# Kernel optimization log

Hardware: AMD Instinct MI355X
Metric: run time of the kernel (lower is better)

## Reference

```python
import jax, jax.numpy as jnp
import numpy as np


def setup_inputs() -> dict:
    key = jax.random.key(0)
    ks = jax.random.split(key, 6)
    B, C, H, W = 4, 512, 64, 64
    Ci = C // 2
    x = jax.random.normal(ks[0], (B, C, H, W), dtype=jnp.float32)
    # 1x1 conv weights (kaiming-ish scale)
    wq = jax.random.normal(ks[1], (Ci, C), dtype=jnp.float32) * np.float32(np.sqrt(2.0 / C))
    wk = jax.random.normal(ks[2], (Ci, C), dtype=jnp.float32) * np.float32(np.sqrt(2.0 / C))
    wv = jax.random.normal(ks[3], (C, C), dtype=jnp.float32) * np.float32(np.sqrt(2.0 / C))
    bq = jnp.zeros((Ci,), jnp.float32)
    bk = jnp.zeros((Ci,), jnp.float32)
    bv = jnp.zeros((C,), jnp.float32)
    gamma_pam = jax.random.uniform(ks[4], (1,), dtype=jnp.float32)
    gamma_cam = jax.random.uniform(ks[5], (1,), dtype=jnp.float32)
    return {"x": x, "wq": wq, "bq": bq, "wk": wk, "bk": bk,
            "wv": wv, "bv": bv, "gamma_pam": gamma_pam, "gamma_cam": gamma_cam}


def reference(x, wq, bq, wk, bk, wv, bv, gamma_pam, gamma_cam):
    B, C, H, W = x.shape
    N = H * W
    xf = x.reshape(B, C, N)  # [B,C,N]

    # ---- PAM (position attention) ----
    q = jnp.einsum('oc,bcn->bon', wq, xf) + bq[None, :, None]  # [B,C/2,N]
    k = jnp.einsum('oc,bcn->bon', wk, xf) + bk[None, :, None]  # [B,C/2,N]
    v = jnp.einsum('oc,bcn->bon', wv, xf) + bv[None, :, None]  # [B,C,N]
    # energy[b,i,j] = sum_c q[b,c,i] k[b,c,j] / sqrt(C)
    energy = jnp.einsum('bci,bcj->bij', q, k) / jnp.sqrt(jnp.float32(C))
    attn = jax.nn.softmax(energy, axis=-1) / jnp.float32(N)  # [B,N,N]
    # out[b,c,i] = sum_j v[b,c,j] * attn[i,j]
    pam_out = jnp.einsum('bcj,bij->bci', v, attn)
    sa = jnp.tanh(gamma_pam[0] * pam_out + xf)  # [B,C,N]

    # ---- CAM (channel attention) on sa ----
    energy_c = jnp.einsum('bcn,bdn->bcd', sa, sa) / jnp.sqrt(jnp.float32(N))  # [B,C,C]
    energy_new = jnp.max(energy_c, axis=-1, keepdims=True) - energy_c
    attn_c = jax.nn.softmax(energy_new, axis=-1) / jnp.float32(C)
    cam_out = jnp.einsum('bcd,bdn->bcn', attn_c, sa)
    out = gamma_cam[0] * cam_out + sa
    return out.reshape(B, C, H, W)
```

## Files before the change

kernel.cpp:

```cpp
#include <hip/hip_runtime.h>

#define B_ 4
#define C_ 512
#define CI_ 256
#define N_ 4096
#define SCALE_PAM 0.04419417382415922f
#define SCALE_CAM (1.0f/64.0f)
#define SHIFT_PAM 8.0f

typedef float v4f __attribute__((ext_vector_type(4)));
typedef short v8s __attribute__((ext_vector_type(8)));

__device__ __forceinline__ unsigned short f2bf(float f) {
  unsigned int u = __float_as_uint(f);
  u = (u + 0x7FFFu + ((u >> 16) & 1u)) >> 16;
  return (unsigned short)u;
}
__device__ __forceinline__ float bf2f(unsigned short s) {
  return __uint_as_float(((unsigned int)s) << 16);
}
__device__ __forceinline__ v8s ld8(const unsigned short* p) {
  v8s r; *(int4*)&r = *(const int4*)p; return r;
}
__device__ __forceinline__ v4f mfma16(v8s a, v8s b, v4f c) {
  return __builtin_amdgcn_mfma_f32_16x16x32_bf16(a, b, c, 0, 0, 0);
}

__global__ __launch_bounds__(256) void k_wb(const float* __restrict__ wq,
                                            const float* __restrict__ wk,
                                            const float* __restrict__ wv,
                                            unsigned short* __restrict__ w_pk) {
  int u = blockIdx.x * 256 + threadIdx.x;
  int blk = u >> 6, wi = (u & 63) * 8;
  int r = (blk >> 4) * 16 + (wi >> 5);
  int k = (blk & 15) * 32 + (wi & 31);
  const float* src = (r < 256) ? &wq[r * 512 + k]
                   : (r < 512) ? &wk[(r - 256) * 512 + k]
                               : &wv[(r - 512) * 512 + k];
  float4 f0 = *(const float4*)src, f1 = *(const float4*)(src + 4);
  ushort4 o0 = { f2bf(f0.x), f2bf(f0.y), f2bf(f0.z), f2bf(f0.w) };
  ushort4 o1 = { f2bf(f1.x), f2bf(f1.y), f2bf(f1.z), f2bf(f1.w) };
  *(ushort4*)&w_pk[u * 8] = o0;
  *(ushort4*)&w_pk[u * 8 + 4] = o1;
}

__global__ __launch_bounds__(256) void k_xT(const float* __restrict__ x,
                                            unsigned short* __restrict__ x_pk) {
  const int b = blockIdx.z, c0 = blockIdx.y * 64, n0 = blockIdx.x * 64;
  const int t = threadIdx.x;
  __shared__ unsigned short ts[64 * 72];
  const int cl = t >> 2, nseg = (t & 3) * 16;
  const float* xr = x + ((size_t)b * C_ + c0 + cl) * N_ + n0 + nseg;
#pragma unroll
  for (int k = 0; k < 4; ++k) {
    float4 f = *(const float4*)(xr + k * 4);
    ts[(nseg + k * 4 + 0) * 72 + cl] = f2bf(f.x);
    ts[(nseg + k * 4 + 1) * 72 + cl] = f2bf(f.y);
    ts[(nseg + k * 4 + 2) * 72 + cl] = f2bf(f.z);
    ts[(nseg + k * 4 + 3) * 72 + cl] = f2bf(f.w);
  }
  __syncthreads();
  unsigned short* dst = x_pk + (size_t)b * N_ * C_;
#pragma unroll
  for (int u = t; u < 512; u += 256) {
    int blk = u >> 6, wi = (u & 63) * 8;
    int rl = (blk >> 1) * 16 + (wi >> 5);
    int kl = (blk & 1) * 32 + (wi & 31);
    int gr = n0 + rl, gk = c0 + kl;
    size_t go = ((size_t)(gr >> 4) * 16 + (gk >> 5)) * 512 + (gr & 15) * 32 + (gk & 31);
    *(int4*)&dst[go] = *(int4*)&ts[rl * 72 + kl];
  }
}

__global__ __launch_bounds__(512) void k_qkv(
    const unsigned short* __restrict__ w_pk, const unsigned short* __restrict__ x_pk,
    const float* __restrict__ bq, const float* __restrict__ bk, const float* __restrict__ bv,
    unsigned short* __restrict__ q_pk, unsigned short* __restrict__ k_pk,
    unsigned short* __restrict__ v_pk) {
  const int b = blockIdx.z, o0 = blockIdx.y * 128, n0 = blockIdx.x * 128;
  const int t = threadIdx.x, wave = t >> 6, lane = t & 63;
  const int la = lane & 15, quad = lane >> 4;
  const int ow = wave & 1, nw = wave >> 1;
  const int lanelin = la * 32 + quad * 8;
  const unsigned short* xpb = x_pk + (size_t)b * N_ * C_;
  __shared__ unsigned short tp[128 * 136];

  v4f acc[4][2];
#pragma unroll
  for (int i = 0; i < 4; ++i)
#pragma unroll
    for (int j = 0; j < 2; ++j) acc[i][j] = (v4f){0.f, 0.f, 0.f, 0.f};

  const int ar16 = (o0 + ow * 64) >> 4;
  const int br16 = (n0 + nw * 32) >> 4;
#pragma unroll 4
  for (int s = 0; s < 16; ++s) {
    v8s b0 = ld8(&xpb[((size_t)(br16 + 0) * 16 + s) * 512 + lanelin]);
    v8s b1 = ld8(&xpb[((size_t)(br16 + 1) * 16 + s) * 512 + lanelin]);
#pragma unroll
    for (int oi = 0; oi < 4; ++oi) {
      v8s a = ld8(&w_pk[((size_t)(ar16 + oi) * 16 + s) * 512 + lanelin]);
      acc[oi][0] = mfma16(a, b0, acc[oi][0]);
      acc[oi][1] = mfma16(a, b1, acc[oi][1]);
    }
  }

  if (o0 >= 512) {
#pragma unroll
    for (int oi = 0; oi < 4; ++oi)
#pragma unroll
      for (int nj = 0; nj < 2; ++nj)
#pragma unroll
        for (int r = 0; r < 4; ++r) {
          int cl = ow * 64 + oi * 16 + quad * 4 + r;
          int nl = nw * 32 + nj * 16 + la;
          tp[cl * 136 + nl] = f2bf(acc[oi][nj][r] + bv[o0 - 512 + cl]);
        }
    __syncthreads();
    unsigned short* dst = v_pk + (size_t)b * C_ * N_;
#pragma unroll
    for (int u = t; u < 2048; u += 512) {
      int blk = u >> 6, wi = (u & 63) * 8;
      int rl = (blk >> 2) * 16 + (wi >> 5);
      int kl = (blk & 3) * 32 + (wi & 31);
      int gr = (o0 - 512) + rl, gk = n0 + kl;
      size_t go = ((size_t)(gr >> 4) * 128 + (gk >> 5)) * 512 + (gr & 15) * 32 + (gk & 31);
      *(int4*)&dst[go] = *(int4*)&tp[rl * 136 + kl];
    }
  } else {
    const float* bias = (o0 < 256) ? bq : bk;
#pragma unroll
    for (int oi = 0; oi < 4; ++oi)
#pragma unroll
      for (int nj = 0; nj < 2; ++nj)
#pragma unroll
        for (int r = 0; r < 4; ++r) {
          int ol = ow * 64 + oi * 16 + quad * 4 + r;
          int nl = nw * 32 + nj * 16 + la;
          tp[nl * 136 + ol] = f2bf(acc[oi][nj][r] + bias[(o0 & 255) + ol]);
        }
    __syncthreads();
    unsigned short* dst = ((o0 < 256) ? q_pk : k_pk) + (size_t)b * N_ * CI_;
#pragma unroll
    for (int u = t; u < 2048; u += 512) {
      int blk = u >> 6, wi = (u & 63) * 8;
      int rl = (blk >> 2) * 16 + (wi >> 5);
      int kl = (blk & 3) * 32 + (wi & 31);
      int gr = n0 + rl, gk = (o0 & 255) + kl;
      size_t go = ((size_t)(gr >> 4) * 8 + (gk >> 5)) * 512 + (gr & 15) * 32 + (gk & 31);
      *(int4*)&dst[go] = *(int4*)&tp[rl * 136 + kl];
    }
  }
}

__device__ __forceinline__ void kstage(const unsigned short* g, unsigned short* l, int t) {
  __builtin_amdgcn_global_load_lds(
      (const __attribute__((address_space(1))) void*)(g + (size_t)t * 8),
      (__attribute__((address_space(3))) void*)(l + t * 8), 16, 0, 0);
  __builtin_amdgcn_global_load_lds(
      (const __attribute__((address_space(1))) void*)(g + 8192 + (size_t)t * 8),
      (__attribute__((address_space(3))) void*)(l + 8192 + t * 8), 16, 0, 0);
}

__global__ __launch_bounds__(1024) void k_pam(
    const unsigned short* __restrict__ q_pk, const unsigned short* __restrict__ k_pk,
    const unsigned short* __restrict__ v_pk,
    float* __restrict__ acc_part, float* __restrict__ l_part) {
  const int blk = blockIdx.x;
  const int b = (blk & 7) >> 1, jh = blk & 1, i0 = (blk >> 3) * 64;
  const int t = threadIdx.x, wave = t >> 6, lane = t & 63;
  const int la = lane & 15, quad = lane >> 4;
  const int iw = wave & 3, jw = wave >> 2;
  const int cb = wave * 32;
  const int lanelin = la * 32 + quad * 8;

  __shared__ unsigned short kls[3][16384];
  __shared__ unsigned short pa[2][4096];
  __shared__ float l_lds[64];
  if (t < 64) l_lds[t] = 0.f;

  const unsigned short* qpk = q_pk + (size_t)b * N_ * CI_;
  const unsigned short* kpk = k_pk + (size_t)b * N_ * CI_;
  const unsigned short* vpk = v_pk + (size_t)b * C_ * N_;

  v8s qf[8];
  {
    const unsigned short* qb = qpk + ((size_t)((i0 >> 4) + iw) * 8) * 512 + lanelin;
#pragma unroll
    for (int s = 0; s < 8; ++s) qf[s] = ld8(qb + s * 512);
  }

  v4f acc[2][4];
#pragma unroll
  for (int ct = 0; ct < 2; ++ct)
#pragma unroll
    for (int it = 0; it < 4; ++it) acc[ct][it] = (v4f){0.f, 0.f, 0.f, 0.f};
  float lsum[4] = {0.f, 0.f, 0.f, 0.f};

  const int jbeg = jh * 2048, jend = jbeg + 2048;
  kstage(kpk + (size_t)(jbeg >> 4) * 4096, kls[0], t);
  kstage(kpk + (size_t)((jbeg + 64) >> 4) * 4096, kls[1], t);
  asm volatile("s_waitcnt vmcnt(2)" ::: "memory");
  __builtin_amdgcn_s_barrier();
  __builtin_amdgcn_sched_barrier(0);

  int pb = 0;
  for (int step = 0; step < 32; ++step) {
    const int j0 = jbeg + step * 64;
    v8s vf[2][2];
#pragma unroll
    for (int ct = 0; ct < 2; ++ct)
#pragma unroll
      for (int ks = 0; ks < 2; ++ks)
        vf[ct][ks] = ld8(&vpk[((size_t)((cb >> 4) + ct) * 128 + (j0 >> 5) + ks) * 512 + lanelin]);
    __builtin_amdgcn_sched_barrier(0);
    int jn = j0 + 128; if (jn >= jend) jn = jbeg;
    kstage(kpk + (size_t)(jn >> 4) * 4096, kls[(step + 2) % 3], t);
    __builtin_amdgcn_sched_barrier(0);
    const unsigned short* kb = &kls[step % 3][jw * 4096 + lanelin];
    v4f sA = (v4f){0.f, 0.f, 0.f, 0.f}, sB = sA;
#pragma unroll
    for (int sh = 0; sh < 4; ++sh) {
      sA = mfma16(qf[sh], ld8(kb + sh * 512), sA);
      sB = mfma16(qf[sh + 4], ld8(kb + (sh + 4) * 512), sB);
    }
#pragma unroll
    for (int r = 0; r < 4; ++r) {
      float p = __expf((sA[r] + sB[r]) * SCALE_PAM - SHIFT_PAM);
      lsum[r] += p;
      int row = iw * 16 + quad * 4 + r;
      pa[pb][((row << 6) + jw * 16 + la) ^ ((row & 7) << 3)] = f2bf(p);
    }
    __builtin_amdgcn_sched_barrier(0);
    asm volatile("s_waitcnt lgkmcnt(0) vmcnt(6)" ::: "memory");
    __builtin_amdgcn_s_barrier();
    __builtin_amdgcn_sched_barrier(0);
    __builtin_amdgcn_s_setprio(1);
#pragma unroll
    for (int it = 0; it < 4; ++it) {
      const int row = it * 16 + la;
      const int sw = (row & 7) << 3;
#pragma unroll
      for (int ks = 0; ks < 2; ++ks) {
        v8s pf; *(int4*)&pf = *(const int4*)&pa[pb][((row << 6) + ks * 32 + quad * 8) ^ sw];
#pragma unroll
        for (int ct = 0; ct < 2; ++ct)
          acc[ct][it] = mfma16(vf[ct][ks], pf, acc[ct][it]);
      }
    }
    __builtin_amdgcn_s_setprio(0);
    pb ^= 1;
  }

#pragma unroll
  for (int r = 0; r < 4; ++r) {
    float v = lsum[r];
    v += __shfl_xor(v, 1); v += __shfl_xor(v, 2);
    v += __shfl_xor(v, 4); v += __shfl_xor(v, 8);
    if (la == 0) atomicAdd(&l_lds[iw * 16 + quad * 4 + r], v);
  }
  __syncthreads();
  if (t < 64) l_part[((size_t)jh * B_ + b) * N_ + i0 + t] = l_lds[t];

  float* ap = acc_part + ((size_t)jh * B_ + b) * C_ * N_;
#pragma unroll
  for (int ct = 0; ct < 2; ++ct)
#pragma unroll
    for (int it = 0; it < 4; ++it)
#pragma unroll
      for (int r = 0; r < 4; ++r)
        ap[(size_t)(cb + ct * 16 + quad * 4 + r) * N_ + i0 + it * 16 + la] = acc[ct][it][r];
}

__global__ __launch_bounds__(256) void k_combine(
    const float* __restrict__ acc_part, const float* __restrict__ l_part,
    const float* __restrict__ x, const float* __restrict__ gamma_pam,
    unsigned short* __restrict__ sa_pk, unsigned short* __restrict__ saT_pk) {
  const int b = blockIdx.z, c0 = blockIdx.y * 64, n0 = blockIdx.x * 64;
  const int t = threadIdx.x;
  const int cl = t >> 2, nseg = (t & 3) * 16;
  __shared__ unsigned short ts[64 * 72];
  const float gpv = gamma_pam[0];
  const size_t rowoff = ((size_t)b * C_ + c0 + cl) * N_ + n0 + nseg;
  const float* a0 = acc_part + rowoff;
  const float* a1 = acc_part + (size_t)B_ * C_ * N_ + rowoff;
  const float* xr = x + rowoff;
  const float* l0 = l_part + (size_t)b * N_ + n0 + nseg;
  const float* l1 = l_part + ((size_t)B_ + b) * N_ + n0 + nseg;
  unsigned short sv[16];
#pragma unroll
  for (int k = 0; k < 4; ++k) {
    float4 p4 = *(const float4*)(a0 + k * 4);
    float4 q4 = *(const float4*)(a1 + k * 4);
    float4 x4 = *(const float4*)(xr + k * 4);
    float4 u4 = *(const float4*)(l0 + k * 4);
    float4 w4 = *(const float4*)(l1 + k * 4);
    sv[k * 4 + 0] = f2bf(tanhf(fmaf(gpv, (p4.x + q4.x) / ((u4.x + w4.x) * (float)N_), x4.x)));
    sv[k * 4 + 1] = f2bf(tanhf(fmaf(gpv, (p4.y + q4.y) / ((u4.y + w4.y) * (float)N_), x4.y)));
    sv[k * 4 + 2] = f2bf(tanhf(fmaf(gpv, (p4.z + q4.z) / ((u4.z + w4.z) * (float)N_), x4.z)));
    sv[k * 4 + 3] = f2bf(tanhf(fmaf(gpv, (p4.w + q4.w) / ((u4.w + w4.w) * (float)N_), x4.w)));
  }
#pragma unroll
  for (int k = 0; k < 16; ++k) ts[cl * 72 + nseg + k] = sv[k];
  __syncthreads();
  {
    unsigned short* dst = sa_pk + (size_t)b * C_ * N_;
#pragma unroll
    for (int u = t; u < 512; u += 256) {
      int blk = u >> 6, wi = (u & 63) * 8;
      int rl = (blk >> 1) * 16 + (wi >> 5);
      int kl = (blk & 1) * 32 + (wi & 31);
      int gr = c0 + rl, gk = n0 + kl;
      size_t go = ((size_t)(gr >> 4) * 128 + (gk >> 5)) * 512 + (gr & 15) * 32 + (gk & 31);
      *(int4*)&dst[go] = *(int4*)&ts[rl * 72 + kl];
    }
  }
  __syncthreads();
#pragma unroll
  for (int k = 0; k < 16; ++k) ts[(nseg + k) * 72 + cl] = sv[k];
  __syncthreads();
  {
    unsigned short* dst = saT_pk + (size_t)b * N_ * C_;
#pragma unroll
    for (int u = t; u < 512; u += 256) {
      int blk = u >> 6, wi = (u & 63) * 8;
      int rl = (blk >> 1) * 16 + (wi >> 5);
      int kl = (blk & 1) * 32 + (wi & 31);
      int gr = n0 + rl, gk = c0 + kl;
      size_t go = ((size_t)(gr >> 4) * 16 + (gk >> 5)) * 512 + (gr & 15) * 32 + (gk & 31);
      *(int4*)&dst[go] = *(int4*)&ts[rl * 72 + kl];
    }
  }
}

__global__ __launch_bounds__(256) void k_cam_e(const unsigned short* __restrict__ sa_pk,
                                               float* __restrict__ e_part) {
  const int b = blockIdx.z, ks = blockIdx.y;
  const int c0 = (blockIdx.x & 7) * 64, d0 = (blockIdx.x >> 3) * 64;
  const int t = threadIdx.x, wave = t >> 6, lane = t & 63;
  const int la = lane & 15, quad = lane >> 4;
  const int cw = wave & 1, dw = wave >> 1;
  const int lanelin = la * 32 + quad * 8;
  const unsigned short* sb = sa_pk + (size_t)b * C_ * N_;

  v4f acc[2][2];
#pragma unroll
  for (int i = 0; i < 2; ++i)
#pragma unroll
    for (int j = 0; j < 2; ++j) acc[i][j] = (v4f){0.f, 0.f, 0.f, 0.f};

  const int ar16 = (c0 + cw * 32) >> 4;
  const int br16 = (d0 + dw * 32) >> 4;
#pragma unroll 4
  for (int s = 0; s < 32; ++s) {
    const int k32 = ks * 32 + s;
    v8s a0 = ld8(&sb[((size_t)(ar16 + 0) * 128 + k32) * 512 + lanelin]);
    v8s a1 = ld8(&sb[((size_t)(ar16 + 1) * 128 + k32) * 512 + lanelin]);
    v8s b0 = ld8(&sb[((size_t)(br16 + 0) * 128 + k32) * 512 + lanelin]);
    v8s b1 = ld8(&sb[((size_t)(br16 + 1) * 128 + k32) * 512 + lanelin]);
    acc[0][0] = mfma16(a0, b0, acc[0][0]);
    acc[0][1] = mfma16(a0, b1, acc[0][1]);
    acc[1][0] = mfma16(a1, b0, acc[1][0]);
    acc[1][1] = mfma16(a1, b1, acc[1][1]);
  }
  float* ep = e_part + ((size_t)(ks * B_ + b)) * C_ * C_;
#pragma unroll
  for (int i = 0; i < 2; ++i)
#pragma unroll
    for (int j = 0; j < 2; ++j)
#pragma unroll
      for (int r = 0; r < 4; ++r) {
        int c = c0 + cw * 32 + i * 16 + quad * 4 + r;
        int d = d0 + dw * 32 + j * 16 + la;
        ep[(size_t)c * C_ + d] = acc[i][j][r] * SCALE_CAM;
      }
}

__global__ __launch_bounds__(64) void k_cam_softmax(const float* __restrict__ e_part,
                                                    unsigned short* __restrict__ attn_pk) {
  const int c = blockIdx.x, b = blockIdx.y, lane = threadIdx.x;
  size_t roff = ((size_t)b * C_ + c) * C_;
  float vals[8];
#pragma unroll
  for (int r = 0; r < 8; ++r) {
    int d = lane + r * 64;
    float s = 0.f;
#pragma unroll
    for (int p = 0; p < 4; ++p) s += e_part[(size_t)(p * B_) * C_ * C_ + roff + d];
    vals[r] = s;
  }
  float mn = vals[0];
#pragma unroll
  for (int r = 1; r < 8; ++r) mn = fminf(mn, vals[r]);
#pragma unroll
  for (int m = 32; m >= 1; m >>= 1) mn = fminf(mn, __shfl_xor(mn, m));
  float sum = 0.f;
#pragma unroll
  for (int r = 0; r < 8; ++r) { vals[r] = __expf(mn - vals[r]); sum += vals[r]; }
#pragma unroll
  for (int m = 32; m >= 1; m >>= 1) sum += __shfl_xor(sum, m);
  float sc = (1.0f / (float)C_) / sum;
  unsigned short* ab = attn_pk + (size_t)b * C_ * C_;
#pragma unroll
  for (int r = 0; r < 8; ++r) {
    int d = lane + r * 64;
    size_t go = ((size_t)(c >> 4) * 16 + (d >> 5)) * 512 + (c & 15) * 32 + (d & 31);
    ab[go] = f2bf(vals[r] * sc);
  }
}

__global__ __launch_bounds__(512) void k_cam_out(
    const unsigned short* __restrict__ attn_pk, const unsigned short* __restrict__ saT_pk,
    const unsigned short* __restrict__ sa_pk, const float* __restrict__ gamma_cam,
    float* __restrict__ out) {
  const int b = blockIdx.z, c0 = blockIdx.y * 128, n0 = blockIdx.x * 128;
  const int t = threadIdx.x, wave = t >> 6, lane = t & 63;
  const int la = lane & 15, quad = lane >> 4;
  const int cw = wave & 1, nw = wave >> 1;
  const int lanelin = la * 32 + quad * 8;
  const unsigned short* ab = attn_pk + (size_t)b * C_ * C_;
  const unsigned short* sTb = saT_pk + (size_t)b * N_ * C_;
  const unsigned short* sb = sa_pk + (size_t)b * C_ * N_;

  v4f acc[4][2];
#pragma unroll
  for (int i = 0; i < 4; ++i)
#pragma unroll
    for (int j = 0; j < 2; ++j) acc[i][j] = (v4f){0.f, 0.f, 0.f, 0.f};

  const int ar16 = (c0 + cw * 64) >> 4;
  const int br16 = (n0 + nw * 32) >> 4;
#pragma unroll 4
  for (int s = 0; s < 16; ++s) {
    v8s b0 = ld8(&sTb[((size_t)(br16 + 0) * 16 + s) * 512 + lanelin]);
    v8s b1 = ld8(&sTb[((size_t)(br16 + 1) * 16 + s) * 512 + lanelin]);
#pragma unroll
    for (int ci = 0; ci < 4; ++ci) {
      v8s a = ld8(&ab[((size_t)(ar16 + ci) * 16 + s) * 512 + lanelin]);
      acc[ci][0] = mfma16(a, b0, acc[ci][0]);
      acc[ci][1] = mfma16(a, b1, acc[ci][1]);
    }
  }
  const float gc = gamma_cam[0];
#pragma unroll
  for (int ci = 0; ci < 4; ++ci)
#pragma unroll
    for (int nj = 0; nj < 2; ++nj)
#pragma unroll
      for (int r = 0; r < 4; ++r) {
        int c = c0 + cw * 64 + ci * 16 + quad * 4 + r;
        int n = n0 + nw * 32 + nj * 16 + la;
        size_t pko = ((size_t)(c >> 4) * 128 + (n >> 5)) * 512 + (c & 15) * 32 + (n & 31);
        out[((size_t)b * C_ + c) * N_ + n] = fmaf(gc, acc[ci][nj][r], bf2f(sb[pko]));
      }
}

extern "C" void kernel_launch(void* const* d_in, const int* in_sizes, int n_in,
                              void* d_out, int out_size, void* d_ws, size_t ws_size,
                              hipStream_t stream) {
  const float* x  = (const float*)d_in[0];
  const float* wq = (const float*)d_in[1];
  const float* bq = (const float*)d_in[2];
  const float* wk = (const float*)d_in[3];
  const float* bk = (const float*)d_in[4];
  const float* wv = (const float*)d_in[5];
  const float* bv = (const float*)d_in[6];
  const float* gp = (const float*)d_in[7];
  const float* gc = (const float*)d_in[8];
  float* out = (float*)d_out;

  char* ws = (char*)d_ws;
  unsigned short* x_pk   = (unsigned short*)(ws);
  unsigned short* w_pk   = (unsigned short*)(ws + 16777216);
  unsigned short* q_pk   = (unsigned short*)(ws + 17825792);
  unsigned short* k_pk   = (unsigned short*)(ws + 26214400);
  unsigned short* v_pk   = (unsigned short*)(ws + 34603008);
  float*          acc_p  = (float*)(ws + 51380224);
  float*          l_p    = (float*)(ws + 118489088);
  unsigned short* sa_pk  = (unsigned short*)(ws);
  unsigned short* saT_pk = (unsigned short*)(ws + 17825792);
  float*          ep     = (float*)(ws + 34603008);
  unsigned short* at_pk  = (unsigned short*)(ws + 51380224);

  k_xT<<<dim3(64, 8, B_), 256, 0, stream>>>(x, x_pk);
  k_wb<<<256, 256, 0, stream>>>(wq, wk, wv, w_pk);
  k_qkv<<<dim3(32, 8, B_), 512, 0, stream>>>(w_pk, x_pk, bq, bk, bv, q_pk, k_pk, v_pk);
  k_pam<<<512, 1024, 0, stream>>>(q_pk, k_pk, v_pk, acc_p, l_p);
  k_combine<<<dim3(64, 8, B_), 256, 0, stream>>>(acc_p, l_p, x, gp, sa_pk, saT_pk);
  k_cam_e<<<dim3(64, 4, B_), 256, 0, stream>>>(sa_pk, ep);
  k_cam_softmax<<<dim3(C_, B_), 64, 0, stream>>>(ep, at_pk);
  k_cam_out<<<dim3(32, 4, B_), 512, 0, stream>>>(at_pk, saT_pk, sa_pk, gc, out);
}
```

Measured before the change: 398.8 us.

## Load K fragments directly into registers instead of staging through LDS

Removes the triple-buffered LDS staging of K tiles via global_load_lds and instead has each wave load its K fragments straight from global memory into registers, prefetching the next step's fragments after the QK MFMAs. This removes 96KB of LDS usage and the associated LDS reads. In exchange, the 4 waves that share the same jw each fetch the same K data from global memory, the register footprint grows by 8 vectors, and the vmcnt wait is dropped so ordering is left to the compiler.

```diff
diff --git a/kernel.cpp b/kernel.cpp
--- a/kernel.cpp
+++ b/kernel.cpp
@@ -153,15 +153,6 @@
   }
 }
 
-__device__ __forceinline__ void kstage(const unsigned short* g, unsigned short* l, int t) {
-  __builtin_amdgcn_global_load_lds(
-      (const __attribute__((address_space(1))) void*)(g + (size_t)t * 8),
-      (__attribute__((address_space(3))) void*)(l + t * 8), 16, 0, 0);
-  __builtin_amdgcn_global_load_lds(
-      (const __attribute__((address_space(1))) void*)(g + 8192 + (size_t)t * 8),
-      (__attribute__((address_space(3))) void*)(l + 8192 + t * 8), 16, 0, 0);
-}
-
 __global__ __launch_bounds__(1024) void k_pam(
     const unsigned short* __restrict__ q_pk, const unsigned short* __restrict__ k_pk,
     const unsigned short* __restrict__ v_pk,
@@ -174,7 +165,6 @@
   const int cb = wave * 32;
   const int lanelin = la * 32 + quad * 8;
 
-  __shared__ unsigned short kls[3][16384];
   __shared__ unsigned short pa[2][4096];
   __shared__ float l_lds[64];
   if (t < 64) l_lds[t] = 0.f;
@@ -198,11 +188,13 @@
   float lsum[4] = {0.f, 0.f, 0.f, 0.f};
 
   const int jbeg = jh * 2048, jend = jbeg + 2048;
-  kstage(kpk + (size_t)(jbeg >> 4) * 4096, kls[0], t);
-  kstage(kpk + (size_t)((jbeg + 64) >> 4) * 4096, kls[1], t);
-  asm volatile("s_waitcnt vmcnt(2)" ::: "memory");
-  __builtin_amdgcn_s_barrier();
-  __builtin_amdgcn_sched_barrier(0);
+
+  v8s kf[8];
+  {
+    const unsigned short* kb = kpk + ((size_t)((jbeg >> 4) + jw) * 8) * 512 + lanelin;
+#pragma unroll
+    for (int s = 0; s < 8; ++s) kf[s] = ld8(kb + s * 512);
+  }
 
   int pb = 0;
   for (int step = 0; step < 32; ++step) {
@@ -213,16 +205,17 @@
 #pragma unroll
       for (int ks = 0; ks < 2; ++ks)
         vf[ct][ks] = ld8(&vpk[((size_t)((cb >> 4) + ct) * 128 + (j0 >> 5) + ks) * 512 + lanelin]);
-    __builtin_amdgcn_sched_barrier(0);
-    int jn = j0 + 128; if (jn >= jend) jn = jbeg;
-    kstage(kpk + (size_t)(jn >> 4) * 4096, kls[(step + 2) % 3], t);
-    __builtin_amdgcn_sched_barrier(0);
-    const unsigned short* kb = &kls[step % 3][jw * 4096 + lanelin];
     v4f sA = (v4f){0.f, 0.f, 0.f, 0.f}, sB = sA;
 #pragma unroll
     for (int sh = 0; sh < 4; ++sh) {
-      sA = mfma16(qf[sh], ld8(kb + sh * 512), sA);
-      sB = mfma16(qf[sh + 4], ld8(kb + (sh + 4) * 512), sB);
+      sA = mfma16(qf[sh], kf[sh], sA);
+      sB = mfma16(qf[sh + 4], kf[sh + 4], sB);
+    }
+    {
+      int jn = j0 + 64; if (jn >= jend) jn = jbeg;
+      const unsigned short* kb = kpk + ((size_t)((jn >> 4) + jw) * 8) * 512 + lanelin;
+#pragma unroll
+      for (int s = 0; s < 8; ++s) kf[s] = ld8(kb + s * 512);
     }
 #pragma unroll
     for (int r = 0; r < 4; ++r) {
@@ -232,7 +225,7 @@
       pa[pb][((row << 6) + jw * 16 + la) ^ ((row & 7) << 3)] = f2bf(p);
     }
     __builtin_amdgcn_sched_barrier(0);
-    asm volatile("s_waitcnt lgkmcnt(0) vmcnt(6)" ::: "memory");
+    asm volatile("s_waitcnt lgkmcnt(0)" ::: "memory");
     __builtin_amdgcn_s_barrier();
     __builtin_amdgcn_sched_barrier(0);
     __builtin_amdgcn_s_setprio(1);
```

Result: slower. 848.6 us (+112.8%).

## Drop PAM split-K and fuse combine/tanh epilogue into attention kernel

Applied to the files above, without the earlier changes.

The PAM kernel no longer splits the key dimension across two blocks. Each block now walks all 4096 keys, and the grid is halved to 256 blocks. This lets the normalization, gamma residual, tanh and the bf16 packing of both sa layouts happen in-kernel through LDS staging, which removes the fp32 partial-accumulator round trip through memory and the separate combine launch. The trade-off is half as many blocks (256 on a 256-CU part, one 1024-thread block each) and a serial loop twice as long.

```diff
diff --git a/kernel.cpp b/kernel.cpp
--- a/kernel.cpp
+++ b/kernel.cpp
@@ -164,10 +164,11 @@
 
 __global__ __launch_bounds__(1024) void k_pam(
     const unsigned short* __restrict__ q_pk, const unsigned short* __restrict__ k_pk,
-    const unsigned short* __restrict__ v_pk,
-    float* __restrict__ acc_part, float* __restrict__ l_part) {
+    const unsigned short* __restrict__ v_pk, const float* __restrict__ x,
+    const float* __restrict__ gamma_pam,
+    unsigned short* __restrict__ sa_pk, unsigned short* __restrict__ saT_pk) {
   const int blk = blockIdx.x;
-  const int b = (blk & 7) >> 1, jh = blk & 1, i0 = (blk >> 3) * 64;
+  const int b = blk & 3, i0 = (blk >> 2) * 64;
   const int t = threadIdx.x, wave = t >> 6, lane = t & 63;
   const int la = lane & 15, quad = lane >> 4;
   const int iw = wave & 3, jw = wave >> 2;
@@ -197,16 +198,15 @@
     for (int it = 0; it < 4; ++it) acc[ct][it] = (v4f){0.f, 0.f, 0.f, 0.f};
   float lsum[4] = {0.f, 0.f, 0.f, 0.f};
 
-  const int jbeg = jh * 2048, jend = jbeg + 2048;
-  kstage(kpk + (size_t)(jbeg >> 4) * 4096, kls[0], t);
-  kstage(kpk + (size_t)((jbeg + 64) >> 4) * 4096, kls[1], t);
+  kstage(kpk, kls[0], t);
+  kstage(kpk + (size_t)4 * 4096, kls[1], t);
   asm volatile("s_waitcnt vmcnt(2)" ::: "memory");
   __builtin_amdgcn_s_barrier();
   __builtin_amdgcn_sched_barrier(0);
 
   int pb = 0;
-  for (int step = 0; step < 32; ++step) {
-    const int j0 = jbeg + step * 64;
+  for (int step = 0; step < 64; ++step) {
+    const int j0 = step * 64;
     v8s vf[2][2];
 #pragma unroll
     for (int ct = 0; ct < 2; ++ct)
@@ -214,7 +214,7 @@
       for (int ks = 0; ks < 2; ++ks)
         vf[ct][ks] = ld8(&vpk[((size_t)((cb >> 4) + ct) * 128 + (j0 >> 5) + ks) * 512 + lanelin]);
     __builtin_amdgcn_sched_barrier(0);
-    int jn = j0 + 128; if (jn >= jend) jn = jbeg;
+    int jn = j0 + 128; if (jn >= N_) jn = 0;
     kstage(kpk + (size_t)(jn >> 4) * 4096, kls[(step + 2) % 3], t);
     __builtin_amdgcn_sched_barrier(0);
     const unsigned short* kb = &kls[step % 3][jw * 4096 + lanelin];
@@ -260,75 +260,54 @@
     if (la == 0) atomicAdd(&l_lds[iw * 16 + quad * 4 + r], v);
   }
   __syncthreads();
-  if (t < 64) l_part[((size_t)jh * B_ + b) * N_ + i0 + t] = l_lds[t];
-
-  float* ap = acc_part + ((size_t)jh * B_ + b) * C_ * N_;
+
+  const float gpv = gamma_pam[0];
+  unsigned short* ts = &kls[0][0];
+  unsigned short sv[2][4][4];
 #pragma unroll
   for (int ct = 0; ct < 2; ++ct)
 #pragma unroll
-    for (int it = 0; it < 4; ++it)
-#pragma unroll
-      for (int r = 0; r < 4; ++r)
-        ap[(size_t)(cb + ct * 16 + quad * 4 + r) * N_ + i0 + it * 16 + la] = acc[ct][it][r];
-}
-
-__global__ __launch_bounds__(256) void k_combine(
-    const float* __restrict__ acc_part, const float* __restrict__ l_part,
-    const float* __restrict__ x, const float* __restrict__ gamma_pam,
-    unsigned short* __restrict__ sa_pk, unsigned short* __restrict__ saT_pk) {
-  const int b = blockIdx.z, c0 = blockIdx.y * 64, n0 = blockIdx.x * 64;
-  const int t = threadIdx.x;
-  const int cl = t >> 2, nseg = (t & 3) * 16;
-  __shared__ unsigned short ts[64 * 72];
-  const float gpv = gamma_pam[0];
-  const size_t rowoff = ((size_t)b * C_ + c0 + cl) * N_ + n0 + nseg;
-  const float* a0 = acc_part + rowoff;
-  const float* a1 = acc_part + (size_t)B_ * C_ * N_ + rowoff;
-  const float* xr = x + rowoff;
-  const float* l0 = l_part + (size_t)b * N_ + n0 + nseg;
-  const float* l1 = l_part + ((size_t)B_ + b) * N_ + n0 + nseg;
-  unsigned short sv[16];
-#pragma unroll
-  for (int k = 0; k < 4; ++k) {
-    float4 p4 = *(const float4*)(a0 + k * 4);
-    float4 q4 = *(const float4*)(a1 + k * 4);
-    float4 x4 = *(const float4*)(xr + k * 4);
-    float4 u4 = *(const float4*)(l0 + k * 4);
-    float4 w4 = *(const float4*)(l1 + k * 4);
-    sv[k * 4 + 0] = f2bf(tanhf(fmaf(gpv, (p4.x + q4.x) / ((u4.x + w4.x) * (float)N_), x4.x)));
-    sv[k * 4 + 1] = f2bf(tanhf(fmaf(gpv, (p4.y + q4.y) / ((u4.y + w4.y) * (float)N_), x4.y)));
-    sv[k * 4 + 2] = f2bf(tanhf(fmaf(gpv, (p4.z + q4.z) / ((u4.z + w4.z) * (float)N_), x4.z)));
-    sv[k * 4 + 3] = f2bf(tanhf(fmaf(gpv, (p4.w + q4.w) / ((u4.w + w4.w) * (float)N_), x4.w)));
-  }
-#pragma unroll
-  for (int k = 0; k < 16; ++k) ts[cl * 72 + nseg + k] = sv[k];
+    for (int it = 0; it < 4; ++it) {
+      const int nl = it * 16 + la;
+      const float lv = l_lds[nl] * (float)N_;
+#pragma unroll
+      for (int r = 0; r < 4; ++r) {
+        const int c = cb + ct * 16 + quad * 4 + r;
+        const float xv = x[((size_t)b * C_ + c) * N_ + i0 + nl];
+        const unsigned short h = f2bf(tanhf(fmaf(gpv, acc[ct][it][r] / lv, xv)));
+        sv[ct][it][r] = h;
+        ts[c * 72 + nl] = h;
+      }
+    }
   __syncthreads();
   {
     unsigned short* dst = sa_pk + (size_t)b * C_ * N_;
 #pragma unroll
-    for (int u = t; u < 512; u += 256) {
-      int blk = u >> 6, wi = (u & 63) * 8;
-      int rl = (blk >> 1) * 16 + (wi >> 5);
-      int kl = (blk & 1) * 32 + (wi & 31);
-      int gr = c0 + rl, gk = n0 + kl;
-      size_t go = ((size_t)(gr >> 4) * 128 + (gk >> 5)) * 512 + (gr & 15) * 32 + (gk & 31);
-      *(int4*)&dst[go] = *(int4*)&ts[rl * 72 + kl];
+    for (int u = t; u < 4096; u += 1024) {
+      int c = u >> 3, n8 = (u & 7) * 8;
+      int gn = i0 + n8;
+      size_t go = ((size_t)(c >> 4) * 128 + (gn >> 5)) * 512 + (c & 15) * 32 + (gn & 31);
+      *(int4*)&dst[go] = *(const int4*)&ts[c * 72 + n8];
     }
   }
   __syncthreads();
-#pragma unroll
-  for (int k = 0; k < 16; ++k) ts[(nseg + k) * 72 + cl] = sv[k];
+  unsigned short* ts2 = &kls[0][0];
+#pragma unroll
+  for (int ct = 0; ct < 2; ++ct)
+#pragma unroll
+    for (int it = 0; it < 4; ++it)
+#pragma unroll
+      for (int r = 0; r < 4; ++r)
+        ts2[(it * 16 + la) * 520 + (cb + ct * 16 + quad * 4 + r)] = sv[ct][it][r];
   __syncthreads();
   {
     unsigned short* dst = saT_pk + (size_t)b * N_ * C_;
 #pragma unroll
-    for (int u = t; u < 512; u += 256) {
-      int blk = u >> 6, wi = (u & 63) * 8;
-      int rl = (blk >> 1) * 16 + (wi >> 5);
-      int kl = (blk & 1) * 32 + (wi & 31);
-      int gr = n0 + rl, gk = c0 + kl;
-      size_t go = ((size_t)(gr >> 4) * 16 + (gk >> 5)) * 512 + (gr & 15) * 32 + (gk & 31);
-      *(int4*)&dst[go] = *(int4*)&ts[rl * 72 + kl];
+    for (int u = t; u < 4096; u += 1024) {
+      int nl = u >> 6, c8 = (u & 63) * 8;
+      int gn = i0 + nl;
+      size_t go = ((size_t)(gn >> 4) * 16 + (c8 >> 5)) * 512 + (gn & 15) * 32 + (c8 & 31);
+      *(int4*)&dst[go] = *(const int4*)&ts2[nl * 520 + c8];
     }
   }
 }
@@ -475,18 +454,15 @@
   unsigned short* q_pk   = (unsigned short*)(ws + 17825792);
   unsigned short* k_pk   = (unsigned short*)(ws + 26214400);
   unsigned short* v_pk   = (unsigned short*)(ws + 34603008);
-  float*          acc_p  = (float*)(ws + 51380224);
-  float*          l_p    = (float*)(ws + 118489088);
-  unsigned short* sa_pk  = (unsigned short*)(ws);
-  unsigned short* saT_pk = (unsigned short*)(ws + 17825792);
+  unsigned short* sa_pk  = (unsigned short*)(ws + 51380224);
+  unsigned short* saT_pk = (unsigned short*)(ws + 68157440);
   float*          ep     = (float*)(ws + 34603008);
-  unsigned short* at_pk  = (unsigned short*)(ws + 51380224);
+  unsigned short* at_pk  = (unsigned short*)(ws);
 
   k_xT<<<dim3(64, 8, B_), 256, 0, stream>>>(x, x_pk);
   k_wb<<<256, 256, 0, stream>>>(wq, wk, wv, w_pk);
   k_qkv<<<dim3(32, 8, B_), 512, 0, stream>>>(w_pk, x_pk, bq, bk, bv, q_pk, k_pk, v_pk);
-  k_pam<<<512, 1024, 0, stream>>>(q_pk, k_pk, v_pk, acc_p, l_p);
-  k_combine<<<dim3(64, 8, B_), 256, 0, stream>>>(acc_p, l_p, x, gp, sa_pk, saT_pk);
+  k_pam<<<256, 1024, 0, stream>>>(q_pk, k_pk, v_pk, x, gp, sa_pk, saT_pk);
   k_cam_e<<<dim3(64, 4, B_), 256, 0, stream>>>(sa_pk, ep);
   k_cam_softmax<<<dim3(C_, B_), 64, 0, stream>>>(ep, at_pk);
   k_cam_out<<<dim3(32, 4, B_), 512, 0, stream>>>(at_pk, saT_pk, sa_pk, gc, out);
```

Measured after the change: 360.9 us (median of 2 runs). 9.5% less time.
